# Kernel optimization log

Measured on AMD Instinct MI355X. Metric: run time of the kernel, lower is better.

## Reference

```python
import jax, jax.numpy as jnp
import numpy as np

N = 50000      # nodes
E = 800000     # edges
IN = 128       # in_channels
HID = 128      # hidden_channels
OUT = 40       # out_channels (classes)
L = 2          # num_layers
K = 3          # K_order
H = 1          # num_heads
EPS = 1e-5     # BatchNorm eps


def setup_inputs() -> dict:
    key = jax.random.key(0)
    ks = jax.random.split(key, 10)
    x = jax.random.normal(ks[0], (N, IN), jnp.float32)
    edge_index = jax.random.randint(ks[1], (2, E), 0, N, dtype=jnp.int32)
    def lin(k, sh, fan):
        return jax.random.normal(k, sh, jnp.float32) / np.float32(np.sqrt(fan))
    W_in = lin(ks[2], (IN, HID), IN); b_in = jnp.zeros((HID,), jnp.float32)
    Wq = lin(ks[3], (L, HID, HID * H), HID); bq = jnp.zeros((L, HID * H), jnp.float32)
    Wk = lin(ks[4], (L, HID, HID * H), HID); bk = jnp.zeros((L, HID * H), jnp.float32)
    fc_in = HID * (K + H + 1)  # 640: cat of attn (HID*H) and gnn (HID*(K+1))
    Wfc = lin(ks[5], (L, fc_in, HID), fc_in); bfc = jnp.zeros((L, HID), jnp.float32)
    W_out = lin(ks[6], (HID, OUT), HID); b_out = jnp.zeros((OUT,), jnp.float32)
    bn_g = jnp.ones((L + 1, HID), jnp.float32)
    bn_b = jnp.zeros((L + 1, HID), jnp.float32)
    return dict(x=x, edge_index=edge_index, W_in=W_in, b_in=b_in, Wq=Wq, bq=bq,
                Wk=Wk, bk=bk, Wfc=Wfc, bfc=bfc, W_out=W_out, b_out=b_out,
                bn_g=bn_g, bn_b=bn_b)


def _bn(x, g, b):
    # BatchNorm1d with batch statistics (biased variance), affine params g, b
    m = x.mean(axis=0)
    v = ((x - m) ** 2).mean(axis=0)
    return g * (x - m) * jax.lax.rsqrt(v + EPS) + b


def reference(x, edge_index, W_in, b_in, Wq, bq, Wk, bk, Wfc, bfc, W_out, b_out, bn_g, bn_b):
    row, col = edge_index[0], edge_index[1]
    # symmetric-normalized adjacency: A_hat[col,row] = d[col]^-1/2 * d[row]^-1/2
    deg = jax.ops.segment_sum(jnp.ones((E,), x.dtype), col, num_segments=N)
    dis = jnp.where(deg > 0, deg ** -0.5, 0.0)
    ew = dis[col] * dis[row]  # [E]

    def prop(h):  # out[c] = sum_e ew[e] * h[row[e]] scattered to col[e]
        return jax.ops.segment_sum(ew[:, None] * h[row], col, num_segments=N)

    h = jax.nn.relu(_bn(x @ W_in + b_in, bn_g[0], bn_b[0]))
    for i in range(L):
        # --- global linear attention (kernel='simple', non-blockwise) ---
        q = (h @ Wq[i] + bq[i]).reshape(N, H, HID)
        k = (h @ Wk[i] + bk[i]).reshape(N, H, HID)
        v = jnp.broadcast_to(h[:, None, :], (N, H, HID))
        qn = q / jnp.linalg.norm(q, axis=2, keepdims=True)
        kn = k / jnp.linalg.norm(k, axis=2, keepdims=True)
        kvs = jnp.einsum('lhm,lhd->hmd', kn, v)                 # [H,D,D]
        num = jnp.einsum('nhm,hmd->nhd', qn, kvs) + v.sum(0)    # [N,H,D]
        den = jnp.einsum('nhm,hm->nh', qn, kn.sum(0))[..., None] + jnp.asarray(N, x.dtype)
        x1 = (num / den).reshape(N, H * HID)
        # --- K-hop normalized-adjacency diffusion ---
        xs = [h]
        for _ in range(K):
            xs.append(prop(xs[-1]))
        x2 = jnp.concatenate(xs, axis=1)                         # [N, HID*(K+1)]
        z = jnp.concatenate([x1, x2], axis=1) @ Wfc[i] + bfc[i]
        z = z + h  # residual
        h = jax.nn.relu(_bn(z, bn_g[i + 1], bn_b[i + 1]))
    return h @ W_out + b_out
```

## Files before the change

### kernel.cpp

```cpp
#include <hip/hip_runtime.h>
#include <hip/hip_bf16.h>
#include <math.h>

#define NN 50000
#define NE 800000
#define HD 128
#define EPS_BN 1e-5f

typedef __bf16 bf16_t;
typedef bf16_t bf16x8 __attribute__((ext_vector_type(8)));
typedef bf16_t bf16x4 __attribute__((ext_vector_type(4)));
typedef float f32x4 __attribute__((ext_vector_type(4)));

__global__ void count_edges(const int* __restrict__ col, int* __restrict__ counts, int E) {
    int e = blockIdx.x * 256 + threadIdx.x;
    if (e >= E) return;
    atomicAdd(&counts[col[e]], 1);
}

__global__ void dis_kernel(const int* __restrict__ counts, float* __restrict__ dis, int N) {
    int i = blockIdx.x * 256 + threadIdx.x;
    if (i >= N) return;
    int c = counts[i];
    dis[i] = (c > 0) ? rsqrtf((float)c) : 0.0f;
}

__global__ __launch_bounds__(256) void scan1(const int* __restrict__ counts,
                                             int* __restrict__ offsets,
                                             int* __restrict__ bsum, int n) {
    __shared__ int wsl[4];
    int t = threadIdx.x, lane = t & 63, w = t >> 6;
    int i = blockIdx.x * 256 + t;
    int v = (i < n) ? counts[i] : 0;
    int x = v;
    #pragma unroll
    for (int o = 1; o < 64; o <<= 1) {
        int tt = __shfl_up(x, o, 64);
        if (lane >= o) x += tt;
    }
    if (lane == 63) wsl[w] = x;
    __syncthreads();
    if (t == 0) {
        int s = 0;
        #pragma unroll
        for (int k = 0; k < 4; k++) { int tmp = wsl[k]; wsl[k] = s; s += tmp; }
        bsum[blockIdx.x] = s;
    }
    __syncthreads();
    if (i < n) offsets[i] = x - v + wsl[w];
}

__global__ __launch_bounds__(256) void scan2(int* __restrict__ bsum, int* __restrict__ offsets,
                                             int nb, int n) {
    __shared__ int wsl[4];
    int t = threadIdx.x, lane = t & 63, w = t >> 6;
    int v = (t < nb) ? bsum[t] : 0;
    int x = v;
    #pragma unroll
    for (int o = 1; o < 64; o <<= 1) {
        int tt = __shfl_up(x, o, 64);
        if (lane >= o) x += tt;
    }
    if (lane == 63) wsl[w] = x;
    __syncthreads();
    if (t == 0) {
        int s = 0;
        #pragma unroll
        for (int k = 0; k < 4; k++) { int tmp = wsl[k]; wsl[k] = s; s += tmp; }
    }
    __syncthreads();
    int excl = x - v + wsl[w];
    if (t < nb) bsum[t] = excl;
    if (t == nb - 1) offsets[n] = excl + v;
}

__global__ void scan3(int* __restrict__ offsets, const int* __restrict__ bsum, int n) {
    int i = blockIdx.x * 256 + threadIdx.x;
    if (i < n) offsets[i] += bsum[blockIdx.x];
}

__global__ void scatter_edges2(const int* __restrict__ row, const int* __restrict__ col,
                               const float* __restrict__ dis, const int* __restrict__ offsets,
                               int* __restrict__ cursor, int2* __restrict__ edges, int E) {
    int e = blockIdx.x * 256 + threadIdx.x;
    if (e >= E) return;
    int c = col[e], r = row[e];
    int pos = offsets[c] + atomicAdd(&cursor[c], 1);
    edges[pos] = make_int2(r, __float_as_int(dis[c] * dis[r]));
}

__global__ __launch_bounds__(256) void prop_b2(const int* __restrict__ offsets,
                                               const int2* __restrict__ edges,
                                               const bf16_t* __restrict__ in,
                                               bf16_t* __restrict__ out) {
    int wave = threadIdx.x >> 6;
    int lane = threadIdx.x & 63;
    int half = lane >> 5;
    int ch4 = (lane & 31) * 4;
    int c = blockIdx.x * 4 + wave;
    if (c >= NN) return;
    int s = offsets[c], e = offsets[c + 1];
    float a0 = 0.0f, a1 = 0.0f, a2 = 0.0f, a3 = 0.0f;
    int i = s + half;
    for (; i + 6 < e; i += 8) {
        int2 r0 = edges[i], r1 = edges[i + 2], r2 = edges[i + 4], r3 = edges[i + 6];
        bf16x4 v0 = *(const bf16x4*)(in + ((size_t)r0.x << 7) + ch4);
        bf16x4 v1 = *(const bf16x4*)(in + ((size_t)r1.x << 7) + ch4);
        bf16x4 v2 = *(const bf16x4*)(in + ((size_t)r2.x << 7) + ch4);
        bf16x4 v3 = *(const bf16x4*)(in + ((size_t)r3.x << 7) + ch4);
        float w0 = __int_as_float(r0.y), w1 = __int_as_float(r1.y);
        float w2 = __int_as_float(r2.y), w3 = __int_as_float(r3.y);
        a0 += w0 * (float)v0[0] + w1 * (float)v1[0] + w2 * (float)v2[0] + w3 * (float)v3[0];
        a1 += w0 * (float)v0[1] + w1 * (float)v1[1] + w2 * (float)v2[1] + w3 * (float)v3[1];
        a2 += w0 * (float)v0[2] + w1 * (float)v1[2] + w2 * (float)v2[2] + w3 * (float)v3[2];
        a3 += w0 * (float)v0[3] + w1 * (float)v1[3] + w2 * (float)v2[3] + w3 * (float)v3[3];
    }
    for (; i < e; i += 2) {
        int2 r0 = edges[i];
        bf16x4 v0 = *(const bf16x4*)(in + ((size_t)r0.x << 7) + ch4);
        float w0 = __int_as_float(r0.y);
        a0 += w0 * (float)v0[0];
        a1 += w0 * (float)v0[1];
        a2 += w0 * (float)v0[2];
        a3 += w0 * (float)v0[3];
    }
    a0 += __shfl_xor(a0, 32);
    a1 += __shfl_xor(a1, 32);
    a2 += __shfl_xor(a2, 32);
    a3 += __shfl_xor(a3, 32);
    if (half == 0) {
        bf16x4 o;
        o[0] = (bf16_t)a0; o[1] = (bf16_t)a1; o[2] = (bf16_t)a2; o[3] = (bf16_t)a3;
        *(bf16x4*)(out + ((size_t)c << 7) + ch4) = o;
    }
}

__global__ void wcvt_frag(const float* __restrict__ W, bf16_t* __restrict__ Wp, int nkc) {
    int p = blockIdx.x * 256 + threadIdx.x;
    if (p >= 8 * nkc * 64) return;
    int lane = p & 63;
    int tk = p >> 6;
    int kc = tk % nkc;
    int t = tk / nkc;
    int n = t * 16 + (lane & 15);
    int k0 = kc * 32 + (lane >> 4) * 8;
    bf16x8 f;
    #pragma unroll
    for (int j = 0; j < 8; j++) f[j] = (bf16_t)W[(size_t)(k0 + j) * 128 + n];
    *(bf16x8*)(Wp + (size_t)p * 8) = f;
}

__global__ void wcvt_out(const float* __restrict__ W, bf16_t* __restrict__ Wp) {
    int p = blockIdx.x * 256 + threadIdx.x;
    if (p >= 3 * 4 * 64) return;
    int lane = p & 63;
    int tk = p >> 6;
    int kc = tk & 3;
    int t = tk >> 2;
    int n = t * 16 + (lane & 15);
    int k0 = kc * 32 + (lane >> 4) * 8;
    bf16x8 f;
    #pragma unroll
    for (int j = 0; j < 8; j++) f[j] = (n < 40) ? (bf16_t)W[(size_t)(k0 + j) * 40 + n] : (bf16_t)0.0f;
    *(bf16x8*)(Wp + (size_t)p * 8) = f;
}

__device__ inline bf16x8 loadA(const float* ap) {
    float4 a0 = *(const float4*)ap;
    float4 a1 = *(const float4*)(ap + 4);
    bf16x8 f;
    f[0] = (bf16_t)a0.x; f[1] = (bf16_t)a0.y; f[2] = (bf16_t)a0.z; f[3] = (bf16_t)a0.w;
    f[4] = (bf16_t)a1.x; f[5] = (bf16_t)a1.y; f[6] = (bf16_t)a1.z; f[7] = (bf16_t)a1.w;
    return f;
}
__device__ inline bf16x8 loadA(const bf16_t* ap) { return *(const bf16x8*)ap; }

template <typename T, bool NORM>
__global__ __launch_bounds__(256) void gemm128s(const T* __restrict__ A,
                                                const bf16_t* __restrict__ Wp,
                                                const float* __restrict__ bias,
                                                const float* __restrict__ ksum_p,
                                                float* __restrict__ den_out,
                                                float* __restrict__ sums,
                                                float* __restrict__ sumsq,
                                                float* __restrict__ out,
                                                bf16_t* __restrict__ outb, int N) {
    __shared__ float lsum[128], lsq[128];
    int tid = threadIdx.x;
    int wave = tid >> 6;
    int lane = tid & 63;
    int quad = lane >> 4;
    int l16 = lane & 15;
    int m0 = blockIdx.x * 64 + wave * 16;
    int arow = m0 + l16;

    f32x4 acc[8] = {};
    #pragma unroll
    for (int kc = 0; kc < 4; kc++) {
        bf16x8 afrag = {};
        if (arow < N) afrag = loadA(A + ((size_t)arow << 7) + kc * 32 + quad * 8);
        bf16x8 bfr[8];
        #pragma unroll
        for (int t = 0; t < 8; t++)
            bfr[t] = *(const bf16x8*)(Wp + (size_t)(((t * 4 + kc) * 64) + lane) * 8);
        #pragma unroll
        for (int t = 0; t < 8; t++)
            acc[t] = __builtin_amdgcn_mfma_f32_16x16x32_bf16(afrag, bfr[t], acc[t], 0, 0, 0);
    }
    float vals[8][4];
    #pragma unroll
    for (int t = 0; t < 8; t++) {
        float b = bias ? bias[t * 16 + l16] : 0.0f;
        #pragma unroll
        for (int r = 0; r < 4; r++) vals[t][r] = acc[t][r] + b;
    }
    if (NORM) {
        #pragma unroll
        for (int r = 0; r < 4; r++) {
            float p = 0.0f;
            #pragma unroll
            for (int t = 0; t < 8; t++) p += vals[t][r] * vals[t][r];
            p += __shfl_xor(p, 1);
            p += __shfl_xor(p, 2);
            p += __shfl_xor(p, 4);
            p += __shfl_xor(p, 8);
            float inv = rsqrtf(p);
            #pragma unroll
            for (int t = 0; t < 8; t++) vals[t][r] *= inv;
        }
    }
    if (ksum_p) {
        float kv[8];
        #pragma unroll
        for (int t = 0; t < 8; t++) kv[t] = ksum_p[t * 16 + l16];
        #pragma unroll
        for (int r = 0; r < 4; r++) {
            float dp = 0.0f;
            #pragma unroll
            for (int t = 0; t < 8; t++) dp += vals[t][r] * kv[t];
            dp += __shfl_xor(dp, 1);
            dp += __shfl_xor(dp, 2);
            dp += __shfl_xor(dp, 4);
            dp += __shfl_xor(dp, 8);
            float dv = dp + (float)NN;
            int rr = m0 + quad * 4 + r;
            if (l16 == 0 && rr < N) den_out[rr] = dv;
            float dinv = 1.0f / dv;
            #pragma unroll
            for (int t = 0; t < 8; t++) vals[t][r] *= dinv;
        }
    }
    #pragma unroll
    for (int r = 0; r < 4; r++) {
        int rr = m0 + quad * 4 + r;
        if (rr >= N) continue;
        #pragma unroll
        for (int t = 0; t < 8; t++) {
            int c = t * 16 + l16;
            float v = vals[t][r];
            if (out) out[((size_t)rr << 7) + c] = v;
            if (outb) outb[((size_t)rr << 7) + c] = (bf16_t)v;
        }
    }
    if (sums) {
        if (tid < 128) { lsum[tid] = 0.0f; lsq[tid] = 0.0f; }
        __syncthreads();
        float sp[8] = {}, qp[8] = {};
        #pragma unroll
        for (int r = 0; r < 4; r++) {
            int rr = m0 + quad * 4 + r;
            if (rr >= N) continue;
            #pragma unroll
            for (int t = 0; t < 8; t++) {
                float v = vals[t][r];
                sp[t] += v;
                qp[t] += v * v;
            }
        }
        #pragma unroll
        for (int t = 0; t < 8; t++) {
            sp[t] += __shfl_xor(sp[t], 16);
            sp[t] += __shfl_xor(sp[t], 32);
            qp[t] += __shfl_xor(qp[t], 16);
            qp[t] += __shfl_xor(qp[t], 32);
        }
        if (quad == 0) {
            #pragma unroll
            for (int t = 0; t < 8; t++) {
                atomicAdd(&lsum[t * 16 + l16], sp[t]);
                atomicAdd(&lsq[t * 16 + l16], qp[t]);
            }
        }
        __syncthreads();
        if (tid < 128) {
            atomicAdd(&sums[tid], lsum[tid]);
            atomicAdd(&sumsq[tid], lsq[tid]);
        }
    }
}

__global__ __launch_bounds__(256, 1) void gemm_fc(
    const bf16_t* __restrict__ qn, const bf16_t* __restrict__ s1, const bf16_t* __restrict__ s2,
    const bf16_t* __restrict__ s3, const bf16_t* __restrict__ s4,
    const bf16_t* __restrict__ WpM1, const bf16_t* __restrict__ Wp,
    const float* __restrict__ bvec, const float* __restrict__ bfc,
    const float* __restrict__ den, const bf16_t* __restrict__ resb,
    float* __restrict__ sums, float* __restrict__ sumsq,
    bf16_t* __restrict__ outb, int N) {
    __shared__ float lsum[128], lsq[128];
    const bf16_t* srcs[5] = {qn, s1, s2, s3, s4};
    int tid = threadIdx.x;
    int wave = tid >> 6;
    int lane = tid & 63;
    int quad = lane >> 4;
    int l16 = lane & 15;
    int m0 = blockIdx.x * 128 + wave * 32;

    f32x4 acc[2][8] = {};
    #pragma unroll
    for (int kc = 0; kc < 20; kc++) {
        int s = kc >> 2;
        int klocal = (kc & 3) * 32;
        bf16x8 bfr[8];
        #pragma unroll
        for (int t = 0; t < 8; t++) {
            const bf16_t* bp = (kc < 4) ? WpM1 + (size_t)(((t * 4 + kc) * 64) + lane) * 8
                                        : Wp + (size_t)(((t * 20 + kc) * 64) + lane) * 8;
            bfr[t] = *(const bf16x8*)bp;
        }
        bf16x8 af[2] = {};
        #pragma unroll
        for (int m = 0; m < 2; m++) {
            int arow = m0 + m * 16 + l16;
            if (arow < N)
                af[m] = *(const bf16x8*)(srcs[s] + ((size_t)arow << 7) + klocal + quad * 8);
        }
        #pragma unroll
        for (int t = 0; t < 8; t++) {
            #pragma unroll
            for (int m = 0; m < 2; m++)
                acc[m][t] = __builtin_amdgcn_mfma_f32_16x16x32_bf16(af[m], bfr[t], acc[m][t],
                                                                    0, 0, 0);
        }
    }
    float bv[8], bf[8];
    #pragma unroll
    for (int t = 0; t < 8; t++) {
        bv[t] = bvec[t * 16 + l16];
        bf[t] = bfc[t * 16 + l16];
    }
    if (tid < 128) { lsum[tid] = 0.0f; lsq[tid] = 0.0f; }
    __syncthreads();
    float sp[8] = {}, qp[8] = {};
    #pragma unroll
    for (int m = 0; m < 2; m++) {
        #pragma unroll
        for (int r = 0; r < 4; r++) {
            int rr = m0 + m * 16 + quad * 4 + r;
            if (rr >= N) continue;
            float dinv = 1.0f / den[rr];
            #pragma unroll
            for (int t = 0; t < 8; t++) {
                int c = t * 16 + l16;
                float v = acc[m][t][r] + dinv * bv[t] + bf[t] +
                          (float)resb[((size_t)rr << 7) + c];
                outb[((size_t)rr << 7) + c] = (bf16_t)v;
                sp[t] += v;
                qp[t] += v * v;
            }
        }
    }
    #pragma unroll
    for (int t = 0; t < 8; t++) {
        sp[t] += __shfl_xor(sp[t], 16);
        sp[t] += __shfl_xor(sp[t], 32);
        qp[t] += __shfl_xor(qp[t], 16);
        qp[t] += __shfl_xor(qp[t], 32);
    }
    if (quad == 0) {
        #pragma unroll
        for (int t = 0; t < 8; t++) {
            atomicAdd(&lsum[t * 16 + l16], sp[t]);
            atomicAdd(&lsq[t * 16 + l16], qp[t]);
        }
    }
    __syncthreads();
    if (tid < 128) {
        atomicAdd(&sums[tid], lsum[tid]);
        atomicAdd(&sumsq[tid], lsq[tid]);
    }
}

__global__ __launch_bounds__(256) void out_mfma(const bf16_t* __restrict__ hb,
                                                const bf16_t* __restrict__ Wp,
                                                const float* __restrict__ bias,
                                                float* __restrict__ out, int N) {
    int wave = threadIdx.x >> 6;
    int lane = threadIdx.x & 63;
    int quad = lane >> 4;
    int l16 = lane & 15;
    int m0 = blockIdx.x * 64 + wave * 16;
    int arow = m0 + l16;

    f32x4 acc[3] = {};
    #pragma unroll
    for (int kc = 0; kc < 4; kc++) {
        bf16x8 afrag = {};
        if (arow < N) afrag = *(const bf16x8*)(hb + ((size_t)arow << 7) + kc * 32 + quad * 8);
        #pragma unroll
        for (int t = 0; t < 3; t++) {
            const bf16_t* bp = Wp + (size_t)(((t * 4 + kc) * 64) + lane) * 8;
            acc[t] = __builtin_amdgcn_mfma_f32_16x16x32_bf16(afrag, *(const bf16x8*)bp, acc[t],
                                                             0, 0, 0);
        }
    }
    #pragma unroll
    for (int r = 0; r < 4; r++) {
        int rr = m0 + quad * 4 + r;
        if (rr >= N) continue;
        #pragma unroll
        for (int t = 0; t < 3; t++) {
            int c = t * 16 + l16;
            if (c < 40) out[(size_t)rr * 40 + c] = acc[t][r] + bias[c];
        }
    }
}

__global__ __launch_bounds__(256) void kvs_mfma(const bf16_t* __restrict__ kn,
                                                const bf16_t* __restrict__ v,
                                                float* __restrict__ kvs,
                                                float* __restrict__ ksum,
                                                float* __restrict__ vsum, int N) {
    __shared__ bf16_t Lk[32][132];
    __shared__ bf16_t Lv[32][132];
    __shared__ float lred[256];
    int t = threadIdx.x;
    int wave = t >> 6, lane = t & 63, quad = lane >> 4, l16 = lane & 15;
    int tr = t >> 4, tc = (t & 15) * 8;
    int mbase = wave * 32;
    f32x4 acc[2][8] = {};
    float ks[8] = {}, vs[8] = {};
    for (int base = blockIdx.x * 32; base < N; base += gridDim.x * 32) {
        __syncthreads();
        #pragma unroll
        for (int hh = 0; hh < 2; hh++) {
            int r = hh * 16 + tr;
            int rowi = base + r;
            bf16x8 ck = {}, cv = {};
            if (rowi < N) {
                ck = *(const bf16x8*)(kn + ((size_t)rowi << 7) + tc);
                cv = *(const bf16x8*)(v + ((size_t)rowi << 7) + tc);
            }
            bf16x4 klo, khi, vlo, vhi;
            #pragma unroll
            for (int j = 0; j < 4; j++) {
                klo[j] = ck[j]; khi[j] = ck[j + 4];
                vlo[j] = cv[j]; vhi[j] = cv[j + 4];
                ks[j] += (float)ck[j]; ks[j + 4] += (float)ck[j + 4];
                vs[j] += (float)cv[j]; vs[j + 4] += (float)cv[j + 4];
            }
            *(bf16x4*)&Lk[r][tc] = klo;
            *(bf16x4*)&Lk[r][tc + 4] = khi;
            *(bf16x4*)&Lv[r][tc] = vlo;
            *(bf16x4*)&Lv[r][tc + 4] = vhi;
        }
        __syncthreads();
        bf16x8 af[2], bfr[8];
        #pragma unroll
        for (int mt = 0; mt < 2; mt++)
            #pragma unroll
            for (int j = 0; j < 8; j++) af[mt][j] = Lk[quad * 8 + j][mbase + mt * 16 + l16];
        #pragma unroll
        for (int tt = 0; tt < 8; tt++)
            #pragma unroll
            for (int j = 0; j < 8; j++) bfr[tt][j] = Lv[quad * 8 + j][tt * 16 + l16];
        #pragma unroll
        for (int mt = 0; mt < 2; mt++)
            #pragma unroll
            for (int tt = 0; tt < 8; tt++)
                acc[mt][tt] = __builtin_amdgcn_mfma_f32_16x16x32_bf16(af[mt], bfr[tt],
                                                                      acc[mt][tt], 0, 0, 0);
    }
    #pragma unroll
    for (int mt = 0; mt < 2; mt++)
        #pragma unroll
        for (int tt = 0; tt < 8; tt++)
            #pragma unroll
            for (int r = 0; r < 4; r++) {
                int m = mbase + mt * 16 + quad * 4 + r;
                int d = tt * 16 + l16;
                atomicAdd(&kvs[m * HD + d], acc[mt][tt][r]);
            }
    lred[t] = 0.0f;
    __syncthreads();
    #pragma unroll
    for (int j = 0; j < 8; j++) {
        atomicAdd(&lred[tc + j], ks[j]);
        atomicAdd(&lred[128 + tc + j], vs[j]);
    }
    __syncthreads();
    if (t < 128) {
        atomicAdd(&ksum[t], lred[t]);
        atomicAdd(&vsum[t], lred[t + 128]);
    }
}

__global__ void m1_pack(const float* __restrict__ kvs, const float* __restrict__ W0,
                        const float* __restrict__ vsum, bf16_t* __restrict__ WpM1,
                        float* __restrict__ bvec) {
    if (blockIdx.x == 64) {
        int c = threadIdx.x;
        if (c < 128) {
            float acc = 0.0f;
            for (int d = 0; d < 128; d++) acc += vsum[d] * W0[d * 128 + c];
            bvec[c] = acc;
        }
        return;
    }
    int idx = blockIdx.x * 256 + threadIdx.x;
    int m = idx >> 7;
    int c = idx & 127;
    float acc = 0.0f;
    for (int d = 0; d < 128; d += 4) {
        float4 k4 = *(const float4*)(kvs + m * 128 + d);
        acc += k4.x * W0[(d + 0) * 128 + c] + k4.y * W0[(d + 1) * 128 + c] +
               k4.z * W0[(d + 2) * 128 + c] + k4.w * W0[(d + 3) * 128 + c];
    }
    int t = c >> 4, l16 = c & 15, kc = m >> 5, quad = (m >> 3) & 3, j = m & 7;
    int lane = quad * 16 + l16;
    WpM1[(size_t)(((t * 4 + kc) * 64) + lane) * 8 + j] = (bf16_t)acc;
}

__global__ void bn_finalize(const float* __restrict__ sums, const float* __restrict__ sumsq,
                            const float* __restrict__ g, const float* __restrict__ b,
                            float* __restrict__ scale, float* __restrict__ shift, int N) {
    int ch = threadIdx.x;
    float m = sums[ch] / (float)N;
    float var = sumsq[ch] / (float)N - m * m;
    float sc = g[ch] * rsqrtf(var + EPS_BN);
    scale[ch] = sc;
    shift[ch] = b[ch] - m * sc;
}

__global__ void bn_apply(const bf16_t* __restrict__ z, bf16_t* __restrict__ hb,
                         const float* __restrict__ scale, const float* __restrict__ shift,
                         int n4) {
    int i = blockIdx.x * blockDim.x + threadIdx.x;
    if (i >= n4) return;
    int c4 = i & 31;
    bf16x4 zv = *(const bf16x4*)(z + (size_t)i * 4);
    float4 sc = ((const float4*)scale)[c4];
    float4 sh = ((const float4*)shift)[c4];
    bf16x4 o;
    o[0] = (bf16_t)fmaxf((float)zv[0] * sc.x + sh.x, 0.0f);
    o[1] = (bf16_t)fmaxf((float)zv[1] * sc.y + sh.y, 0.0f);
    o[2] = (bf16_t)fmaxf((float)zv[2] * sc.z + sh.z, 0.0f);
    o[3] = (bf16_t)fmaxf((float)zv[3] * sc.w + sh.w, 0.0f);
    *(bf16x4*)(hb + (size_t)i * 4) = o;
}

extern "C" void kernel_launch(void* const* d_in, const int* in_sizes, int n_in,
                              void* d_out, int out_size, void* d_ws, size_t ws_size,
                              hipStream_t stream) {
    const float* x = (const float*)d_in[0];
    const int* eidx = (const int*)d_in[1];
    const float* W_in = (const float*)d_in[2];
    const float* b_in = (const float*)d_in[3];
    const float* Wq = (const float*)d_in[4];
    const float* bq = (const float*)d_in[5];
    const float* Wk = (const float*)d_in[6];
    const float* bk = (const float*)d_in[7];
    const float* Wfc = (const float*)d_in[8];
    const float* bfc = (const float*)d_in[9];
    const float* W_out = (const float*)d_in[10];
    const float* b_out = (const float*)d_in[11];
    const float* bn_g = (const float*)d_in[12];
    const float* bn_b = (const float*)d_in[13];
    float* out = (float*)d_out;

    const int N = NN, E = NE;
    const int* rowp = eidx;
    const int* colp = eidx + E;

    char* ws = (char*)d_ws;
    size_t off = 0;
    auto nxt = [&](size_t bytes) -> void* {
        void* p = ws + off;
        off += (bytes + 255) & ~(size_t)255;
        return p;
    };
    int* counts = (int*)nxt((size_t)N * 4);
    int* offsets = (int*)nxt((size_t)(N + 1) * 4);
    int* cursor = (int*)nxt((size_t)N * 4);
    int* bsum = (int*)nxt(1024);
    int2* edges = (int2*)nxt((size_t)E * 8);
    float* dis = (float*)nxt((size_t)N * 4);
    float* den = (float*)nxt((size_t)N * 4);
    float* kvs = (float*)nxt((size_t)HD * HD * 4);
    float* ksum = (float*)nxt((size_t)HD * 4);
    float* vsum = (float*)nxt((size_t)HD * 4);
    float* bnsum = (float*)nxt((size_t)HD * 4);
    float* bnsumsq = (float*)nxt((size_t)HD * 4);
    float* bnscale = (float*)nxt((size_t)HD * 4);
    float* bnshift = (float*)nxt((size_t)HD * 4);
    float* bvec = (float*)nxt((size_t)HD * 4);
    bf16_t* zb = (bf16_t*)nxt((size_t)N * HD * 2);
    bf16_t* hb = (bf16_t*)nxt((size_t)N * HD * 2);
    bf16_t* p1b = (bf16_t*)nxt((size_t)N * HD * 2);
    bf16_t* p2b = (bf16_t*)nxt((size_t)N * HD * 2);
    bf16_t* p3b = (bf16_t*)nxt((size_t)N * HD * 2);
    bf16_t* knb = (bf16_t*)nxt((size_t)N * HD * 2);
    bf16_t* qnb = (bf16_t*)nxt((size_t)N * HD * 2);
    bf16_t* Wp_in = (bf16_t*)nxt((size_t)8 * 4 * 64 * 8 * 2);
    bf16_t* Wp_q = (bf16_t*)nxt((size_t)2 * 8 * 4 * 64 * 8 * 2);
    bf16_t* Wp_k = (bf16_t*)nxt((size_t)2 * 8 * 4 * 64 * 8 * 2);
    bf16_t* Wp_fc = (bf16_t*)nxt((size_t)2 * 8 * 20 * 64 * 8 * 2);
    bf16_t* WpM1 = (bf16_t*)nxt((size_t)8 * 4 * 64 * 8 * 2);
    bf16_t* Wp_out = (bf16_t*)nxt((size_t)3 * 4 * 64 * 8 * 2);

    const int GB = (N + 63) / 64;
    const int GB2 = (N + 127) / 128;
    const int QSZ = HD * HD;
    const int FSZ = 8 * 20 * 64 * 8;
    const int NB = (N + 255) / 256;

    hipMemsetAsync(counts, 0, (size_t)N * 4, stream);
    count_edges<<<(E + 255) / 256, 256, 0, stream>>>(colp, counts, E);
    dis_kernel<<<(N + 255) / 256, 256, 0, stream>>>(counts, dis, N);
    scan1<<<NB, 256, 0, stream>>>(counts, offsets, bsum, N);
    scan2<<<1, 256, 0, stream>>>(bsum, offsets, NB, N);
    scan3<<<NB, 256, 0, stream>>>(offsets, bsum, N);
    hipMemsetAsync(cursor, 0, (size_t)N * 4, stream);
    scatter_edges2<<<(E + 255) / 256, 256, 0, stream>>>(rowp, colp, dis, offsets, cursor,
                                                        edges, E);

    wcvt_frag<<<8, 256, 0, stream>>>(W_in, Wp_in, 4);
    wcvt_frag<<<8, 256, 0, stream>>>(Wq, Wp_q, 4);
    wcvt_frag<<<8, 256, 0, stream>>>(Wq + QSZ, Wp_q + QSZ, 4);
    wcvt_frag<<<8, 256, 0, stream>>>(Wk, Wp_k, 4);
    wcvt_frag<<<8, 256, 0, stream>>>(Wk + QSZ, Wp_k + QSZ, 4);
    wcvt_frag<<<40, 256, 0, stream>>>(Wfc, Wp_fc, 20);
    wcvt_frag<<<40, 256, 0, stream>>>(Wfc + 640 * HD, Wp_fc + FSZ, 20);
    wcvt_out<<<3, 256, 0, stream>>>(W_out, Wp_out);

    hipMemsetAsync(bnsum, 0, 1024, stream);
    gemm128s<float, false><<<GB, 256, 0, stream>>>(x, Wp_in, b_in, nullptr, nullptr, bnsum,
                                                   bnsumsq, nullptr, zb, N);
    bn_finalize<<<1, 128, 0, stream>>>(bnsum, bnsumsq, bn_g, bn_b, bnscale, bnshift, N);
    bn_apply<<<(N * 32 + 255) / 256, 256, 0, stream>>>(zb, hb, bnscale, bnshift, N * 32);

    for (int i = 0; i < 2; i++) {
        const float* bq_i = bq + (size_t)i * HD;
        const float* bk_i = bk + (size_t)i * HD;
        const float* bfc_i = bfc + (size_t)i * HD;
        const float* Wfc_i = Wfc + (size_t)i * 640 * HD;
        bf16_t* Wp_q_i = Wp_q + (size_t)i * QSZ;
        bf16_t* Wp_k_i = Wp_k + (size_t)i * QSZ;
        bf16_t* Wp_fc_i = Wp_fc + (size_t)i * FSZ;

        prop_b2<<<(N + 3) / 4, 256, 0, stream>>>(offsets, edges, hb, p1b);
        prop_b2<<<(N + 3) / 4, 256, 0, stream>>>(offsets, edges, p1b, p2b);
        prop_b2<<<(N + 3) / 4, 256, 0, stream>>>(offsets, edges, p2b, p3b);

        gemm128s<bf16_t, true><<<GB, 256, 0, stream>>>(hb, Wp_k_i, bk_i, nullptr, nullptr,
                                                       nullptr, nullptr, nullptr, knb, N);
        hipMemsetAsync(kvs, 0, 66560, stream);
        kvs_mfma<<<256, 256, 0, stream>>>(knb, hb, kvs, ksum, vsum, N);
        gemm128s<bf16_t, true><<<GB, 256, 0, stream>>>(hb, Wp_q_i, bq_i, ksum, den, nullptr,
                                                       nullptr, nullptr, qnb, N);
        m1_pack<<<65, 256, 0, stream>>>(kvs, Wfc_i, vsum, WpM1, bvec);

        hipMemsetAsync(bnsum, 0, 1024, stream);
        gemm_fc<<<GB2, 256, 0, stream>>>(qnb, hb, p1b, p2b, p3b, WpM1, Wp_fc_i, bvec, bfc_i,
                                         den, hb, bnsum, bnsumsq, zb, N);
        bn_finalize<<<1, 128, 0, stream>>>(bnsum, bnsumsq, bn_g + (size_t)(i + 1) * HD,
                                           bn_b + (size_t)(i + 1) * HD, bnscale, bnshift, N);
        bn_apply<<<(N * 32 + 255) / 256, 256, 0, stream>>>(zb, hb, bnscale, bnshift, N * 32);
    }

    out_mfma<<<GB, 256, 0, stream>>>(hb, Wp_out, b_out, out, N);
}
```

Before: 675.2 us.

## Cut kernel launches by fusing setup, memsets and BN finalize; deepen prop unroll

```diff
diff --git a/kernel.cpp b/kernel.cpp
--- a/kernel.cpp
+++ b/kernel.cpp
@@ -18,20 +18,15 @@
     atomicAdd(&counts[col[e]], 1);
 }
 
-__global__ void dis_kernel(const int* __restrict__ counts, float* __restrict__ dis, int N) {
-    int i = blockIdx.x * 256 + threadIdx.x;
-    if (i >= N) return;
-    int c = counts[i];
-    dis[i] = (c > 0) ? rsqrtf((float)c) : 0.0f;
-}
-
 __global__ __launch_bounds__(256) void scan1(const int* __restrict__ counts,
                                              int* __restrict__ offsets,
-                                             int* __restrict__ bsum, int n) {
+                                             int* __restrict__ bsum,
+                                             float* __restrict__ dis, int n) {
     __shared__ int wsl[4];
     int t = threadIdx.x, lane = t & 63, w = t >> 6;
     int i = blockIdx.x * 256 + t;
     int v = (i < n) ? counts[i] : 0;
+    if (i < n) dis[i] = (v > 0) ? rsqrtf((float)v) : 0.0f;
     int x = v;
     #pragma unroll
     for (int o = 1; o < 64; o <<= 1) {
@@ -102,18 +97,21 @@
     int s = offsets[c], e = offsets[c + 1];
     float a0 = 0.0f, a1 = 0.0f, a2 = 0.0f, a3 = 0.0f;
     int i = s + half;
-    for (; i + 6 < e; i += 8) {
-        int2 r0 = edges[i], r1 = edges[i + 2], r2 = edges[i + 4], r3 = edges[i + 6];
-        bf16x4 v0 = *(const bf16x4*)(in + ((size_t)r0.x << 7) + ch4);
-        bf16x4 v1 = *(const bf16x4*)(in + ((size_t)r1.x << 7) + ch4);
-        bf16x4 v2 = *(const bf16x4*)(in + ((size_t)r2.x << 7) + ch4);
-        bf16x4 v3 = *(const bf16x4*)(in + ((size_t)r3.x << 7) + ch4);
-        float w0 = __int_as_float(r0.y), w1 = __int_as_float(r1.y);
-        float w2 = __int_as_float(r2.y), w3 = __int_as_float(r3.y);
-        a0 += w0 * (float)v0[0] + w1 * (float)v1[0] + w2 * (float)v2[0] + w3 * (float)v3[0];
-        a1 += w0 * (float)v0[1] + w1 * (float)v1[1] + w2 * (float)v2[1] + w3 * (float)v3[1];
-        a2 += w0 * (float)v0[2] + w1 * (float)v1[2] + w2 * (float)v2[2] + w3 * (float)v3[2];
-        a3 += w0 * (float)v0[3] + w1 * (float)v1[3] + w2 * (float)v2[3] + w3 * (float)v3[3];
+    for (; i + 14 < e; i += 16) {
+        int2 r[8];
+        #pragma unroll
+        for (int u = 0; u < 8; u++) r[u] = edges[i + u * 2];
+        bf16x4 v[8];
+        #pragma unroll
+        for (int u = 0; u < 8; u++) v[u] = *(const bf16x4*)(in + ((size_t)r[u].x << 7) + ch4);
+        #pragma unroll
+        for (int u = 0; u < 8; u++) {
+            float w = __int_as_float(r[u].y);
+            a0 += w * (float)v[u][0];
+            a1 += w * (float)v[u][1];
+            a2 += w * (float)v[u][2];
+            a3 += w * (float)v[u][3];
+        }
     }
     for (; i < e; i += 2) {
         int2 r0 = edges[i];
@@ -135,8 +133,9 @@
     }
 }
 
-__global__ void wcvt_frag(const float* __restrict__ W, bf16_t* __restrict__ Wp, int nkc) {
-    int p = blockIdx.x * 256 + threadIdx.x;
+__device__ inline void pack_frag(const float* __restrict__ W, bf16_t* __restrict__ Wp, int nkc,
+                                 int lb) {
+    int p = lb * 256 + threadIdx.x;
     if (p >= 8 * nkc * 64) return;
     int lane = p & 63;
     int tk = p >> 6;
@@ -150,19 +149,41 @@
     *(bf16x8*)(Wp + (size_t)p * 8) = f;
 }
 
-__global__ void wcvt_out(const float* __restrict__ W, bf16_t* __restrict__ Wp) {
-    int p = blockIdx.x * 256 + threadIdx.x;
-    if (p >= 3 * 4 * 64) return;
-    int lane = p & 63;
-    int tk = p >> 6;
-    int kc = tk & 3;
-    int t = tk >> 2;
-    int n = t * 16 + (lane & 15);
-    int k0 = kc * 32 + (lane >> 4) * 8;
-    bf16x8 f;
-    #pragma unroll
-    for (int j = 0; j < 8; j++) f[j] = (n < 40) ? (bf16_t)W[(size_t)(k0 + j) * 40 + n] : (bf16_t)0.0f;
-    *(bf16x8*)(Wp + (size_t)p * 8) = f;
+__global__ void wcvt_all(const float* __restrict__ W_in, const float* __restrict__ Wq,
+                         const float* __restrict__ Wk, const float* __restrict__ Wfc,
+                         const float* __restrict__ W_out, bf16_t* __restrict__ Wp_in,
+                         bf16_t* __restrict__ Wp_q, bf16_t* __restrict__ Wp_k,
+                         bf16_t* __restrict__ Wp_fc, bf16_t* __restrict__ Wp_out,
+                         float* __restrict__ bnsum, float* __restrict__ bnsumsq) {
+    const int QSZ = HD * HD;
+    const int FSZ = 8 * 20 * 64 * 8;
+    int b = blockIdx.x;
+    if (b < 8) { pack_frag(W_in, Wp_in, 4, b); return; }
+    if (b < 16) { pack_frag(Wq, Wp_q, 4, b - 8); return; }
+    if (b < 24) { pack_frag(Wq + QSZ, Wp_q + QSZ, 4, b - 16); return; }
+    if (b < 32) { pack_frag(Wk, Wp_k, 4, b - 24); return; }
+    if (b < 40) { pack_frag(Wk + QSZ, Wp_k + QSZ, 4, b - 32); return; }
+    if (b < 80) { pack_frag(Wfc, Wp_fc, 20, b - 40); return; }
+    if (b < 120) { pack_frag(Wfc + 640 * HD, Wp_fc + FSZ, 20, b - 80); return; }
+    if (b < 123) {
+        int p = (b - 120) * 256 + threadIdx.x;
+        if (p >= 3 * 4 * 64) return;
+        int lane = p & 63;
+        int tk = p >> 6;
+        int kc = tk & 3;
+        int t = tk >> 2;
+        int n = t * 16 + (lane & 15);
+        int k0 = kc * 32 + (lane >> 4) * 8;
+        bf16x8 f;
+        #pragma unroll
+        for (int j = 0; j < 8; j++)
+            f[j] = (n < 40) ? (bf16_t)W_out[(size_t)(k0 + j) * 40 + n] : (bf16_t)0.0f;
+        *(bf16x8*)(Wp_out + (size_t)p * 8) = f;
+        return;
+    }
+    int t = threadIdx.x;
+    if (t < 128) bnsum[t] = 0.0f;
+    else bnsumsq[t - 128] = 0.0f;
 }
 
 __device__ inline bf16x8 loadA(const float* ap) {
@@ -183,10 +204,15 @@
                                                 float* __restrict__ den_out,
                                                 float* __restrict__ sums,
                                                 float* __restrict__ sumsq,
+                                                float* __restrict__ zero_buf, int zero_len,
                                                 float* __restrict__ out,
                                                 bf16_t* __restrict__ outb, int N) {
     __shared__ float lsum[128], lsq[128];
     int tid = threadIdx.x;
+    if (zero_buf && blockIdx.x < 17) {
+        int base = (blockIdx.x * 256 + tid) * 4;
+        if (base < zero_len) *(float4*)(zero_buf + base) = make_float4(0.f, 0.f, 0.f, 0.f);
+    }
     int wave = tid >> 6;
     int lane = tid & 63;
     int quad = lane >> 4;
@@ -507,13 +533,17 @@
 
 __global__ void m1_pack(const float* __restrict__ kvs, const float* __restrict__ W0,
                         const float* __restrict__ vsum, bf16_t* __restrict__ WpM1,
-                        float* __restrict__ bvec) {
+                        float* __restrict__ bvec, float* __restrict__ bnsum,
+                        float* __restrict__ bnsumsq) {
     if (blockIdx.x == 64) {
-        int c = threadIdx.x;
-        if (c < 128) {
+        int t = threadIdx.x;
+        if (t < 128) {
+            bnsum[t] = 0.0f;
             float acc = 0.0f;
-            for (int d = 0; d < 128; d++) acc += vsum[d] * W0[d * 128 + c];
-            bvec[c] = acc;
+            for (int d = 0; d < 128; d++) acc += vsum[d] * W0[d * 128 + t];
+            bvec[t] = acc;
+        } else {
+            bnsumsq[t - 128] = 0.0f;
         }
         return;
     }
@@ -531,31 +561,27 @@
     WpM1[(size_t)(((t * 4 + kc) * 64) + lane) * 8 + j] = (bf16_t)acc;
 }
 
-__global__ void bn_finalize(const float* __restrict__ sums, const float* __restrict__ sumsq,
-                            const float* __restrict__ g, const float* __restrict__ b,
-                            float* __restrict__ scale, float* __restrict__ shift, int N) {
-    int ch = threadIdx.x;
-    float m = sums[ch] / (float)N;
-    float var = sumsq[ch] / (float)N - m * m;
-    float sc = g[ch] * rsqrtf(var + EPS_BN);
-    scale[ch] = sc;
-    shift[ch] = b[ch] - m * sc;
-}
-
-__global__ void bn_apply(const bf16_t* __restrict__ z, bf16_t* __restrict__ hb,
-                         const float* __restrict__ scale, const float* __restrict__ shift,
-                         int n4) {
-    int i = blockIdx.x * blockDim.x + threadIdx.x;
+__global__ void bn_apply2(const bf16_t* __restrict__ z, bf16_t* __restrict__ hb,
+                          const float* __restrict__ sums, const float* __restrict__ sumsq,
+                          const float* __restrict__ g, const float* __restrict__ bb, int n4) {
+    __shared__ float sc[128], sh[128];
+    int t = threadIdx.x;
+    if (t < 128) {
+        float m = sums[t] / (float)NN;
+        float var = sumsq[t] / (float)NN - m * m;
+        float s = g[t] * rsqrtf(var + EPS_BN);
+        sc[t] = s;
+        sh[t] = bb[t] - m * s;
+    }
+    __syncthreads();
+    int i = blockIdx.x * 256 + t;
     if (i >= n4) return;
-    int c4 = i & 31;
+    int c4 = (i & 31) * 4;
     bf16x4 zv = *(const bf16x4*)(z + (size_t)i * 4);
-    float4 sc = ((const float4*)scale)[c4];
-    float4 sh = ((const float4*)shift)[c4];
     bf16x4 o;
-    o[0] = (bf16_t)fmaxf((float)zv[0] * sc.x + sh.x, 0.0f);
-    o[1] = (bf16_t)fmaxf((float)zv[1] * sc.y + sh.y, 0.0f);
-    o[2] = (bf16_t)fmaxf((float)zv[2] * sc.z + sh.z, 0.0f);
-    o[3] = (bf16_t)fmaxf((float)zv[3] * sc.w + sh.w, 0.0f);
+    #pragma unroll
+    for (int j = 0; j < 4; j++)
+        o[j] = (bf16_t)fmaxf((float)zv[j] * sc[c4 + j] + sh[c4 + j], 0.0f);
     *(bf16x4*)(hb + (size_t)i * 4) = o;
 }
 
@@ -590,8 +616,8 @@
         return p;
     };
     int* counts = (int*)nxt((size_t)N * 4);
+    int* cursor = (int*)nxt((size_t)N * 4);
     int* offsets = (int*)nxt((size_t)(N + 1) * 4);
-    int* cursor = (int*)nxt((size_t)N * 4);
     int* bsum = (int*)nxt(1024);
     int2* edges = (int2*)nxt((size_t)E * 8);
     float* dis = (float*)nxt((size_t)N * 4);
@@ -601,8 +627,6 @@
     float* vsum = (float*)nxt((size_t)HD * 4);
     float* bnsum = (float*)nxt((size_t)HD * 4);
     float* bnsumsq = (float*)nxt((size_t)HD * 4);
-    float* bnscale = (float*)nxt((size_t)HD * 4);
-    float* bnshift = (float*)nxt((size_t)HD * 4);
     float* bvec = (float*)nxt((size_t)HD * 4);
     bf16_t* zb = (bf16_t*)nxt((size_t)N * HD * 2);
     bf16_t* hb = (bf16_t*)nxt((size_t)N * HD * 2);
@@ -624,30 +648,21 @@
     const int FSZ = 8 * 20 * 64 * 8;
     const int NB = (N + 255) / 256;
 
-    hipMemsetAsync(counts, 0, (size_t)N * 4, stream);
+    hipMemsetAsync(counts, 0, (size_t)2 * ((N * 4 + 255) & ~255), stream);
     count_edges<<<(E + 255) / 256, 256, 0, stream>>>(colp, counts, E);
-    dis_kernel<<<(N + 255) / 256, 256, 0, stream>>>(counts, dis, N);
-    scan1<<<NB, 256, 0, stream>>>(counts, offsets, bsum, N);
+    scan1<<<NB, 256, 0, stream>>>(counts, offsets, bsum, dis, N);
     scan2<<<1, 256, 0, stream>>>(bsum, offsets, NB, N);
     scan3<<<NB, 256, 0, stream>>>(offsets, bsum, N);
-    hipMemsetAsync(cursor, 0, (size_t)N * 4, stream);
     scatter_edges2<<<(E + 255) / 256, 256, 0, stream>>>(rowp, colp, dis, offsets, cursor,
                                                         edges, E);
 
-    wcvt_frag<<<8, 256, 0, stream>>>(W_in, Wp_in, 4);
-    wcvt_frag<<<8, 256, 0, stream>>>(Wq, Wp_q, 4);
-    wcvt_frag<<<8, 256, 0, stream>>>(Wq + QSZ, Wp_q + QSZ, 4);
-    wcvt_frag<<<8, 256, 0, stream>>>(Wk, Wp_k, 4);
-    wcvt_frag<<<8, 256, 0, stream>>>(Wk + QSZ, Wp_k + QSZ, 4);
-    wcvt_frag<<<40, 256, 0, stream>>>(Wfc, Wp_fc, 20);
-    wcvt_frag<<<40, 256, 0, stream>>>(Wfc + 640 * HD, Wp_fc + FSZ, 20);
-    wcvt_out<<<3, 256, 0, stream>>>(W_out, Wp_out);
-
-    hipMemsetAsync(bnsum, 0, 1024, stream);
+    wcvt_all<<<124, 256, 0, stream>>>(W_in, Wq, Wk, Wfc, W_out, Wp_in, Wp_q, Wp_k, Wp_fc,
+                                      Wp_out, bnsum, bnsumsq);
+
     gemm128s<float, false><<<GB, 256, 0, stream>>>(x, Wp_in, b_in, nullptr, nullptr, bnsum,
-                                                   bnsumsq, nullptr, zb, N);
-    bn_finalize<<<1, 128, 0, stream>>>(bnsum, bnsumsq, bn_g, bn_b, bnscale, bnshift, N);
-    bn_apply<<<(N * 32 + 255) / 256, 256, 0, stream>>>(zb, hb, bnscale, bnshift, N * 32);
+                                                   bnsumsq, nullptr, 0, nullptr, zb, N);
+    bn_apply2<<<(N * 32 + 255) / 256, 256, 0, stream>>>(zb, hb, bnsum, bnsumsq, bn_g, bn_b,
+                                                        N * 32);
 
     for (int i = 0; i < 2; i++) {
         const float* bq_i = bq + (size_t)i * HD;
@@ -663,19 +678,19 @@
         prop_b2<<<(N + 3) / 4, 256, 0, stream>>>(offsets, edges, p2b, p3b);
 
         gemm128s<bf16_t, true><<<GB, 256, 0, stream>>>(hb, Wp_k_i, bk_i, nullptr, nullptr,
-                                                       nullptr, nullptr, nullptr, knb, N);
-        hipMemsetAsync(kvs, 0, 66560, stream);
+                                                       nullptr, nullptr, kvs, HD * HD + 2 * HD,
+                                                       nullptr, knb, N);
         kvs_mfma<<<256, 256, 0, stream>>>(knb, hb, kvs, ksum, vsum, N);
         gemm128s<bf16_t, true><<<GB, 256, 0, stream>>>(hb, Wp_q_i, bq_i, ksum, den, nullptr,
-                                                       nullptr, nullptr, qnb, N);
-        m1_pack<<<65, 256, 0, stream>>>(kvs, Wfc_i, vsum, WpM1, bvec);
-
-        hipMemsetAsync(bnsum, 0, 1024, stream);
+                                                       nullptr, nullptr, 0, nullptr, qnb, N);
+        m1_pack<<<65, 256, 0, stream>>>(kvs, Wfc_i, vsum, WpM1, bvec, bnsum, bnsumsq);
+
         gemm_fc<<<GB2, 256, 0, stream>>>(qnb, hb, p1b, p2b, p3b, WpM1, Wp_fc_i, bvec, bfc_i,
                                          den, hb, bnsum, bnsumsq, zb, N);
-        bn_finalize<<<1, 128, 0, stream>>>(bnsum, bnsumsq, bn_g + (size_t)(i + 1) * HD,
-                                           bn_b + (size_t)(i + 1) * HD, bnscale, bnshift, N);
-        bn_apply<<<(N * 32 + 255) / 256, 256, 0, stream>>>(zb, hb, bnscale, bnshift, N * 32);
+        bn_apply2<<<(N * 32 + 255) / 256, 256, 0, stream>>>(zb, hb, bnsum, bnsumsq,
+                                                            bn_g + (size_t)(i + 1) * HD,
+                                                            bn_b + (size_t)(i + 1) * HD,
+                                                            N * 32);
     }
 
     out_mfma<<<GB, 256, 0, stream>>>(hb, Wp_out, b_out, out, N);
```

After: 698.5 us. 1.03x slower.
